# Kernel optimization log

Hardware: AMD Instinct MI355X
Metric: run time of the kernel (lower is better)

## Reference

```python
import jax, jax.numpy as jnp
import numpy as np

N = 50000      # nodes
E = 800000     # edges (avg degree 16)
F_IN = 256     # input feature dim
H, D = 4, 32   # heads, per-head dim
HD = H * D
K = 25000      # SAGPool keeps ceil(0.5*N) nodes
C = 2          # classes
SLOPE = 0.4
NEG = -1e9

def _gat(x, src, dst, valid, n, W, b, al, ar):
    # DGL GATConv: fc -> per-head attn logits -> edge softmax over dst -> weighted sum
    h = (x @ W).reshape(-1, H, D)                      # [n,H,D]
    el = jnp.einsum('nhd,hd->nh', h, al)
    er = jnp.einsum('nhd,hd->nh', h, ar)
    e = jax.nn.leaky_relu(el[src] + er[dst], SLOPE)    # [E,H]
    e = jnp.where(valid[:, None], e, NEG)
    m = jnp.maximum(jax.ops.segment_max(e, dst, num_segments=n), NEG)
    ex = jnp.exp(e - m[dst]) * valid[:, None].astype(x.dtype)
    s = jax.ops.segment_sum(ex, dst, num_segments=n)
    alpha = ex / jnp.maximum(s[dst], 1e-16)            # [E,H] edge softmax
    out = jax.ops.segment_sum(alpha[:, :, None] * h[src], dst, num_segments=n)
    return out + b.reshape(1, H, D), alpha

def _sagpool(x, src, dst, valid, n, k, Wc, bc):
    # score = GraphConv(in,1) with symmetric norm; keep top-k nodes, scale by tanh(score)
    vf = valid.astype(x.dtype)
    deg_o = jnp.maximum(jax.ops.segment_sum(vf, src, num_segments=n), 1.0)
    deg_i = jnp.maximum(jax.ops.segment_sum(vf, dst, num_segments=n), 1.0)
    h = (x @ Wc) * (deg_o ** -0.5)[:, None]
    agg = jax.ops.segment_sum(h[src] * vf[:, None], dst, num_segments=n)
    score = (agg * (deg_i ** -0.5)[:, None] + bc)[:, 0]   # [n]
    vals, perm = jax.lax.top_k(score, k)
    xk = x[perm] * jnp.tanh(vals)[:, None]                # [k,F]
    new_id = jnp.full((n,), -1, jnp.int32).at[perm].set(jnp.arange(k, dtype=jnp.int32))
    ns, nd = new_id[src], new_id[dst]
    nv = valid & (ns >= 0) & (nd >= 0)                    # edges fully inside subgraph
    return xk, jnp.where(nv, ns, 0), jnp.where(nv, nd, 0), nv

def setup_inputs():
    key = jax.random.key(0)
    k = jax.random.split(key, 18)
    rn = lambda i, shape, scale: jax.random.normal(k[i], shape, jnp.float32) * scale
    return {
        "feature": rn(0, (N, F_IN), 1.0),
        "strength": jax.random.uniform(k[1], (E,), dtype=jnp.float32),
        "W0": rn(2, (F_IN, HD), F_IN ** -0.5), "b0": jnp.zeros((HD,), jnp.float32),
        "al0": rn(3, (H, D), 0.1), "ar0": rn(4, (H, D), 0.1),
        "Wc0": rn(5, (HD, 1), HD ** -0.5), "bc0": jnp.zeros((1,), jnp.float32),
        "W1": rn(6, (HD, HD), HD ** -0.5), "b1": jnp.zeros((HD,), jnp.float32),
        "al1": rn(7, (H, D), 0.1), "ar1": rn(8, (H, D), 0.1),
        "gate_W": rn(9, (D, 1), D ** -0.5), "gate_b": jnp.zeros((1,), jnp.float32),
        "cls_W": rn(10, (D, C), D ** -0.5), "cls_b": jnp.zeros((C,), jnp.float32),
        "src": jax.random.randint(k[11], (E,), 0, N, dtype=jnp.int32),
        "dst": jax.random.randint(k[12], (E,), 0, N, dtype=jnp.int32),
    }

def reference(feature, strength, W0, b0, al0, ar0, Wc0, bc0, W1, b1, al1, ar1,
              gate_W, gate_b, cls_W, cls_b, src, dst):
    valid0 = jnp.ones((E,), bool)
    h0, _ = _gat(feature, src, dst, valid0, N, W0, b0, al0, ar0)
    x = h0.reshape(N, HD)                                  # flatten(1)
    x1, s1, d1, v1 = _sagpool(x, src, dst, valid0, N, K, Wc0, bc0)
    h1, atten = _gat(x1, s1, d1, v1, K, W1, b1, al1, ar1)  # get_attention=True
    strength1 = strength * v1.astype(strength.dtype)       # edata carried into subgraph (masked)
    res = h1.mean(axis=1)                                  # [K,D] mean over heads
    gate = jax.nn.softmax(res @ gate_W + gate_b, axis=0)   # [K,1] GlobalAttentionPooling
    readout = jnp.sum(gate * res, axis=0, keepdims=True)   # [1,D]
    lbl_pred = readout @ cls_W + cls_b                     # [1,C]
    return (readout, lbl_pred, atten, strength1)
```

## Files before the change

### kernel.cpp

```cpp
#include <hip/hip_runtime.h>
#include <stdint.h>

#define NN 50000
#define EE 800000
#define FIN 256
#define HD 128
#define DD 32
#define KK 25000
#define SLOPEF 0.4f
#define NEGF (-1e9f)
#define ATT_OFF 34
#define STR_OFF (34 + EE * 4)
#define CW 128

#define BCH 32
#define EPC (EE / BCH)

__device__ __forceinline__ unsigned fkey(float x) {
    unsigned u = __float_as_uint(x);
    return (u & 0x80000000u) ? ~u : (u | 0x80000000u);
}
__device__ __forceinline__ float unfkey(unsigned k) {
    unsigned u = (k & 0x80000000u) ? (k ^ 0x80000000u) : ~k;
    return __uint_as_float(u);
}
__device__ __forceinline__ float lrelu(float v) { return v > 0.f ? v : SLOPEF * v; }

struct P {
    const float *feature, *strength, *W0, *b0, *al0, *ar0, *Wc0, *bc0;
    const float *W1, *b1, *al1, *ar1, *gW, *gb, *cW, *cb;
    const int *src, *dst;
    double *Zacc, *racc;
    int *cnt;
    unsigned *gmaxk, *rs;
    unsigned *binsHi, *binsLo;
    unsigned *keys;
    unsigned char *degc_i, *degc_o, *degc1;
    unsigned *cb0, *cb1;
    int *dsum;
    int *ens, *end_;
    int *csr_src, *rank, *off0, *off1, *sel, *slot, *list, *bsum, *boff;
    float *z0, *el0, *er0, *q4, *m0f, *s0f, *b0wc, *hc, *score, *xk, *z1;
    float *el1, *er1, *m1f, *s1f, *res, *g, *tscale;
    float *out;
};

#define BM 128
#define BN 64
#define BK 16
__device__ void gemm_body(
    const float* __restrict__ A, const float* __restrict__ B, float* __restrict__ C,
    int M, int Kd,
    const float* __restrict__ al, const float* __restrict__ ar,
    float* __restrict__ el, float* __restrict__ er,
    const float* __restrict__ Wc, float* __restrict__ q4,
    int bx, int by) {
    __shared__ float As[BK][BM + 4];
    __shared__ float Bs[BK][BN];
    int bm = by * BM, bn = bx * BN;
    int tid = threadIdx.x;
    int tr = tid >> 4, tc = tid & 15;
    int lrow = tid >> 1;
    int arow = (bm + lrow < M) ? (bm + lrow) : -1;
    float acc[8][4] = {};
    for (int k0 = 0; k0 < Kd; k0 += BK) {
        {
            int col = (tid & 1) << 3;
            float4 v0 = {0.f,0.f,0.f,0.f}, v1 = {0.f,0.f,0.f,0.f};
            if (arow >= 0) {
                const float* ap = A + (size_t)arow * Kd + k0 + col;
                v0 = *(const float4*)ap; v1 = *(const float4*)(ap + 4);
            }
            As[col + 0][lrow] = v0.x; As[col + 1][lrow] = v0.y;
            As[col + 2][lrow] = v0.z; As[col + 3][lrow] = v0.w;
            As[col + 4][lrow] = v1.x; As[col + 5][lrow] = v1.y;
            As[col + 6][lrow] = v1.z; As[col + 7][lrow] = v1.w;
        }
        {
            int kr = tid >> 4, col = (tid & 15) << 2;
            float4 v = *(const float4*)(B + (size_t)(k0 + kr) * HD + bn + col);
            *(float4*)&Bs[kr][col] = v;
        }
        __syncthreads();
#pragma unroll
        for (int kk = 0; kk < BK; kk++) {
            float a[8], b[4];
#pragma unroll
            for (int i = 0; i < 8; i++) a[i] = As[kk][tr * 8 + i];
#pragma unroll
            for (int j = 0; j < 4; j++) b[j] = Bs[kk][tc * 4 + j];
#pragma unroll
            for (int i = 0; i < 8; i++)
#pragma unroll
                for (int j = 0; j < 4; j++) acc[i][j] = fmaf(a[i], b[j], acc[i][j]);
        }
        __syncthreads();
    }
#pragma unroll
    for (int i = 0; i < 8; i++) {
        int gr = bm + tr * 8 + i;
        if (gr < M) {
            float4 v = {acc[i][0], acc[i][1], acc[i][2], acc[i][3]};
            *(float4*)(C + (size_t)gr * HD + bn + tc * 4) = v;
        }
    }
    int head = bx * 2 + (tc >> 3);
    int dbase = (tc & 7) * 4;
    const float* alh = al + head * 32 + dbase;
    const float* arh = ar + head * 32 + dbase;
    float a0 = alh[0], a1 = alh[1], a2 = alh[2], a3 = alh[3];
    float r0 = arh[0], r1 = arh[1], r2 = arh[2], r3 = arh[3];
    float w0 = 0.f, w1 = 0.f, w2 = 0.f, w3 = 0.f;
    if (Wc) {
        const float* wch = Wc + head * 32 + dbase;
        w0 = wch[0]; w1 = wch[1]; w2 = wch[2]; w3 = wch[3];
    }
#pragma unroll
    for (int i = 0; i < 8; i++) {
        int gr = bm + tr * 8 + i;
        float pe = acc[i][0]*a0 + acc[i][1]*a1 + acc[i][2]*a2 + acc[i][3]*a3;
        float pr = acc[i][0]*r0 + acc[i][1]*r1 + acc[i][2]*r2 + acc[i][3]*r3;
        float pq = acc[i][0]*w0 + acc[i][1]*w1 + acc[i][2]*w2 + acc[i][3]*w3;
#pragma unroll
        for (int o = 1; o < 8; o <<= 1) {
            pe += __shfl_xor(pe, o); pr += __shfl_xor(pr, o); pq += __shfl_xor(pq, o);
        }
        if ((tc & 7) == 0 && gr < M) {
            el[gr * 4 + head] = pe; er[gr * 4 + head] = pr;
            if (Wc) q4[gr * 4 + head] = pq;
        }
    }
}

__global__ __launch_bounds__(256) void k_count0(P p) {
    __shared__ unsigned hist[NN / 4];
    int blk = blockIdx.x;
    int isD = blk < BCH;
    int c = isD ? blk : blk - BCH;
    for (int w = threadIdx.x; w < NN / 4; w += 256) hist[w] = 0u;
    __syncthreads();
    int j0 = c * EPC, j1 = j0 + EPC;
    if (isD) {
        for (int e = j0 + (int)threadIdx.x; e < j1; e += 256) {
            int d = p.dst[e];
            unsigned sh = (unsigned)(d & 3) * 8u;
            unsigned old = atomicAdd(&hist[d >> 2], 1u << sh);
            p.rank[e] = (int)((old >> sh) & 0xffu);
        }
    } else {
        for (int e = j0 + (int)threadIdx.x; e < j1; e += 256) {
            int s = p.src[e];
            atomicAdd(&hist[s >> 2], 1u << ((unsigned)(s & 3) * 8u));
        }
    }
    __syncthreads();
    unsigned* o32 = (unsigned*)((isD ? p.degc_i : p.degc_o) + (size_t)c * NN);
    for (int w = threadIdx.x; w < NN / 4; w += 256) o32[w] = hist[w];
}

__global__ __launch_bounds__(256) void k_count1(P p) {
    __shared__ unsigned hist[KK / 4];
    int c = blockIdx.x;
    for (int w = threadIdx.x; w < KK / 4; w += 256) hist[w] = 0u;
    __syncthreads();
    int j0 = c * EPC, j1 = j0 + EPC;
    for (int e = j0 + (int)threadIdx.x; e < j1; e += 256) {
        int d = p.end_[e];
        if (d >= 0) {
            unsigned sh = (unsigned)(d & 3) * 8u;
            unsigned old = atomicAdd(&hist[d >> 2], 1u << sh);
            p.rank[e] = (int)((old >> sh) & 0xffu);
        }
    }
    __syncthreads();
    unsigned* o32 = (unsigned*)(p.degc1 + (size_t)c * KK);
    for (int w = threadIdx.x; w < KK / 4; w += 256) o32[w] = hist[w];
}

__global__ void k_emap(P p) {
    int e = blockIdx.x * blockDim.x + threadIdx.x;
    if (e >= EE) return;
    int ns = p.slot[p.src[e]], nd = p.slot[p.dst[e]];
    if (ns < 0) nd = -1;
    p.ens[e] = ns;
    p.end_[e] = nd;
}

__global__ __launch_bounds__(256) void k_bsum(const unsigned char* __restrict__ deg,
                                              int* __restrict__ bsum, int n, int nn) {
    int i = blockIdx.x * 256 + threadIdx.x;
    int v = 0;
    if (i < n) {
#pragma unroll
        for (int c = 0; c < BCH; c++) v += deg[(size_t)c * nn + i];
    }
    int lane = threadIdx.x & 63, w = threadIdx.x >> 6;
    __shared__ int ws[4];
#pragma unroll
    for (int o = 1; o < 64; o <<= 1) v += __shfl_xor(v, o);
    if (lane == 0) ws[w] = v;
    __syncthreads();
    if (threadIdx.x == 0) bsum[blockIdx.x] = ws[0] + ws[1] + ws[2] + ws[3];
}
__global__ __launch_bounds__(256) void k_bscan(const int* __restrict__ bsum, int nb,
                                               int* __restrict__ boff,
                                               int* __restrict__ off, int n) {
    __shared__ int ws[4];
    __shared__ int wo[5];
    int t = threadIdx.x;
    int v = (t < nb) ? bsum[t] : 0;
    int lane = t & 63, w = t >> 6;
    int incl = v;
    for (int o = 1; o < 64; o <<= 1) { int u = __shfl_up(incl, o); if (lane >= o) incl += u; }
    if (lane == 63) ws[w] = incl;
    __syncthreads();
    if (t == 0) { int a = 0; for (int i = 0; i < 4; i++) { wo[i] = a; a += ws[i]; } wo[4] = a; }
    __syncthreads();
    if (t < nb) boff[t] = wo[w] + incl - v;
    if (t == 0) off[n] = wo[4];
}
__global__ __launch_bounds__(256) void k_fscan0(P p) {
    __shared__ int ws[4];
    __shared__ int wo[4];
    int i = blockIdx.x * 256 + threadIdx.x;
    int v = 0;
    if (i < NN) {
#pragma unroll
        for (int c = 0; c < BCH; c++) v += p.degc_i[(size_t)c * NN + i];
    }
    int lane = threadIdx.x & 63, w = threadIdx.x >> 6;
    int incl = v;
    for (int o = 1; o < 64; o <<= 1) { int u = __shfl_up(incl, o); if (lane >= o) incl += u; }
    if (lane == 63) ws[w] = incl;
    __syncthreads();
    if (threadIdx.x == 0) { int a = 0; for (int k = 0; k < 4; k++) { wo[k] = a; a += ws[k]; } }
    __syncthreads();
    if (i < NN) {
        int base = p.boff[blockIdx.x] + wo[w] + incl - v;
        p.off0[i] = base;
        unsigned run = (unsigned)base;
        int s = 0;
#pragma unroll
        for (int c = 0; c < BCH; c++) {
            p.cb0[(size_t)c * NN + i] = run;
            run += p.degc_i[(size_t)c * NN + i];
            s += p.degc_o[(size_t)c * NN + i];
        }
        p.dsum[i] = s;
    }
}
__global__ __launch_bounds__(256) void k_fscan1(P p) {
    __shared__ int ws[4];
    __shared__ int wo[4];
    int i = blockIdx.x * 256 + threadIdx.x;
    int v = 0;
    if (i < KK) {
#pragma unroll
        for (int c = 0; c < BCH; c++) v += p.degc1[(size_t)c * KK + i];
    }
    int lane = threadIdx.x & 63, w = threadIdx.x >> 6;
    int incl = v;
    for (int o = 1; o < 64; o <<= 1) { int u = __shfl_up(incl, o); if (lane >= o) incl += u; }
    if (lane == 63) ws[w] = incl;
    __syncthreads();
    if (threadIdx.x == 0) { int a = 0; for (int k = 0; k < 4; k++) { wo[k] = a; a += ws[k]; } }
    __syncthreads();
    if (i < KK) {
        int base = p.boff[blockIdx.x] + wo[w] + incl - v;
        p.off1[i] = base;
        unsigned run = (unsigned)base;
#pragma unroll
        for (int c = 0; c < BCH; c++) {
            p.cb1[(size_t)c * KK + i] = run;
            run += p.degc1[(size_t)c * KK + i];
        }
    }
}

#define G0B 782
#define GB_E 3125
__global__ __launch_bounds__(256) void k_g0sc(P p) {
    int blk = blockIdx.x;
    if (blk < G0B) {
        gemm_body(p.feature, p.W0, p.z0, NN, FIN, p.al0, p.ar0, p.el0, p.er0,
                  p.Wc0, p.q4, blk & 1, blk >> 1);
    } else if (blk < G0B + GB_E) {
        int e = (blk - G0B) * 256 + threadIdx.x;
        if (e < EE) {
            int c = e / EPC;
            int d = p.dst[e];
            unsigned pos = p.cb0[(size_t)c * NN + d] + (unsigned)p.rank[e];
            p.csr_src[pos] = p.src[e];
        }
    } else {
        int l = threadIdx.x;
        if (l < 64) {
            float t = p.b0[l] * p.Wc0[l] + p.b0[l + 64] * p.Wc0[l + 64];
#pragma unroll
            for (int o = 1; o < 64; o <<= 1) t += __shfl_xor(t, o);
            if (l == 0) p.b0wc[0] = t;
        }
    }
}

#define G1B 392
__global__ __launch_bounds__(256) void k_g1sc(P p) {
    int blk = blockIdx.x;
    if (blk < G1B) {
        gemm_body(p.xk, p.W1, p.z1, KK, HD, p.al1, p.ar1, p.el1, p.er1,
                  nullptr, nullptr, blk & 1, blk >> 1);
    } else {
        int e = (blk - G1B) * 256 + threadIdx.x;
        if (e < EE) {
            int d = p.end_[e];
            if (d >= 0) {
                int c = e / EPC;
                unsigned pos = p.cb1[(size_t)c * KK + d] + (unsigned)p.rank[e];
                p.csr_src[pos] = p.ens[e];
            }
        }
    }
}

__global__ __launch_bounds__(256) void k_fgatlite(
    const int* __restrict__ off, const int* __restrict__ csrs,
    const float* __restrict__ el, const float* __restrict__ er,
    const float* __restrict__ q4, const int* __restrict__ dsum,
    const float* __restrict__ b0wc,
    float* __restrict__ hc, float* __restrict__ m0f, float* __restrict__ s0f) {
    int wv = threadIdx.x >> 6, lane = threadIdx.x & 63;
    int v = blockIdx.x * 4 + wv;
    int b = off[v], e = off[v + 1], deg = e - b;
    int h = lane >> 4, sub = lane & 15;
    float erh = er[(size_t)v * 4 + h];
    float m = NEGF;
    for (int li = sub; li < deg; li += 16) {
        int s = csrs[b + li];
        m = fmaxf(m, lrelu(el[(size_t)s * 4 + h] + erh));
    }
#pragma unroll
    for (int o = 1; o < 16; o <<= 1) m = fmaxf(m, __shfl_xor(m, o));
    float ssum = 0.f, hq = 0.f;
    for (int li = sub; li < deg; li += 16) {
        int s = csrs[b + li];
        float ex = expf(lrelu(el[(size_t)s * 4 + h] + erh) - m);
        ssum += ex;
        hq = fmaf(ex, q4[(size_t)s * 4 + h], hq);
    }
#pragma unroll
    for (int o = 1; o < 16; o <<= 1) { ssum += __shfl_xor(ssum, o); hq += __shfl_xor(hq, o); }
    if (sub == 0) { m0f[v * 4 + h] = m; s0f[v * 4 + h] = ssum; }
    float t = hq / fmaxf(ssum, 1e-16f);
    t += __shfl_xor(t, 16);
    t += __shfl_xor(t, 32);
    if (lane == 0)
        hc[v] = (t + b0wc[0]) / sqrtf(fmaxf((float)dsum[v], 1.f));
}

__global__ __launch_bounds__(256) void k_fgatx(
    const int* __restrict__ list, const float* __restrict__ tscale,
    const int* __restrict__ off, const int* __restrict__ csrs,
    const float* __restrict__ el, const float* __restrict__ er,
    const float* __restrict__ m0f, const float* __restrict__ s0f,
    const float* __restrict__ z, const float* __restrict__ b0,
    float* __restrict__ xk) {
    __shared__ int ssrc[4][CW];
    __shared__ float sexp[4][CW][4];
    int wv = threadIdx.x >> 6, lane = threadIdx.x & 63;
    int i = blockIdx.x * 4 + wv;
    int v = list[i];
    int b = off[v], e = off[v + 1], deg = e - b;
    int h = lane >> 4, sub = lane & 15;
    float erh = er[(size_t)v * 4 + h];
    float mh = m0f[v * 4 + h];
    for (int li = sub; li < deg; li += 16) {
        int s = csrs[b + li];
        if (h == 0 && li < CW) ssrc[wv][li] = s;
        if (li < CW) sexp[wv][li][h] = expf(lrelu(el[(size_t)s * 4 + h] + erh) - mh);
    }
    __syncthreads();
    int h0 = lane >> 5, h1 = h0 + 2;
    float s0 = s0f[v * 4 + h0], s1 = s0f[v * 4 + h1];
    float m0 = m0f[v * 4 + h0], m1 = m0f[v * 4 + h1];
    float er0v = er[(size_t)v * 4 + h0], er1v = er[(size_t)v * 4 + h1];
    int c0 = lane, c1 = lane + 64;
    float acc0 = 0.f, acc1 = 0.f;
    for (int li = 0; li < deg; li++) {
        int s; float w0, w1;
        if (li < CW) {
            s = ssrc[wv][li];
            w0 = sexp[wv][li][h0]; w1 = sexp[wv][li][h1];
        } else {
            s = csrs[b + li];
            w0 = expf(lrelu(el[(size_t)s * 4 + h0] + er0v) - m0);
            w1 = expf(lrelu(el[(size_t)s * 4 + h1] + er1v) - m1);
        }
        int su = __builtin_amdgcn_readfirstlane(s);
        const float* zr = z + (size_t)su * HD;
        acc0 = fmaf(w0, zr[c0], acc0);
        acc1 = fmaf(w1, zr[c1], acc1);
    }
    float ts = tscale[i];
    float* xr = xk + (size_t)i * HD;
    xr[c0] = (acc0 / fmaxf(s0, 1e-16f) + b0[c0]) * ts;
    xr[c1] = (acc1 / fmaxf(s1, 1e-16f) + b0[c1]) * ts;
}

__global__ void k_score(P p) {
    int v = blockIdx.x * blockDim.x + threadIdx.x;
    if (v >= NN) return;
    int b = p.off0[v], en = p.off0[v + 1];
    float acc = 0.f;
    for (int i = b; i < en; i++) acc += p.hc[p.csr_src[i]];
    float dg = fmaxf((float)(en - b), 1.f);
    float sc = acc / sqrtf(dg) + p.bc0[0];
    p.score[v] = sc;
    p.keys[v] = fkey(sc);
}

__global__ void k_hist2(P p, int level) {
    int v = blockIdx.x * blockDim.x + threadIdx.x;
    if (v >= NN) return;
    unsigned key = p.keys[v];
    if (level == 0) atomicAdd(&p.binsHi[key >> 16], 1u);
    else if ((key >> 16) == p.rs[2]) atomicAdd(&p.binsLo[key & 0xFFFFu], 1u);
}
__global__ __launch_bounds__(1024) void k_rsel2(P p, int level) {
    const unsigned* bins = level ? p.binsLo : p.binsHi;
    int K = level ? (int)p.rs[3] : KK;
    __shared__ unsigned wsm[16];
    __shared__ unsigned wpre[17];
    int t = threadIdx.x;
    unsigned base = (unsigned)t * 64;
    const uint4* b4 = (const uint4*)(bins + base);
    unsigned S = 0;
#pragma unroll
    for (int i = 0; i < 16; i++) {
        uint4 u = b4[i];
        S += u.x + u.y + u.z + u.w;
    }
    int lane = t & 63, w = t >> 6;
    unsigned val = S;
    for (int o = 1; o < 64; o <<= 1) { unsigned u = __shfl_up(val, o); if (lane >= o) val += u; }
    if (lane == 63) wsm[w] = val;
    __syncthreads();
    if (t == 0) { unsigned a = 0; for (int i = 0; i < 16; i++) { wpre[i] = a; a += wsm[i]; } wpre[16] = a; }
    __syncthreads();
    unsigned incl = wpre[w] + val;
    unsigned running = wpre[16] - incl;
    for (int i = 63; i >= 0; i--) {
        unsigned c = bins[base + i];
        unsigned above = running;
        running += c;
        if ((int)above < K && (int)running >= K) {
            if (level == 0) { p.rs[2] = base + (unsigned)i; p.rs[3] = (unsigned)(K - (int)above); }
            else { p.rs[0] = (p.rs[2] << 16) | (base + (unsigned)i); p.rs[1] = (unsigned)(K - (int)above); }
        }
    }
}
__global__ void k_sel(P p) {
    int v = blockIdx.x * blockDim.x + threadIdx.x;
    if (v >= NN) return;
    p.sel[v] = (p.keys[v] > p.rs[0]) ? 1 : 0;
}
__global__ __launch_bounds__(1024) void k_ties(P p) {
    __shared__ int base;
    __shared__ int wsums[16];
    unsigned pivot = p.rs[0];
    int need = (int)p.rs[1];
    if (threadIdx.x == 0) base = 0;
    __syncthreads();
    for (int st = 0; st < NN; st += 1024) {
        int v = st + (int)threadIdx.x;
        int flag = (v < NN && p.keys[v] == pivot) ? 1 : 0;
        unsigned long long m = __ballot(flag);
        int lane = threadIdx.x & 63, w = threadIdx.x >> 6;
        int pre = __popcll(m & ((1ull << lane) - 1ull));
        if (lane == 0) wsums[w] = __popcll(m);
        __syncthreads();
        int woff = 0;
        for (int i = 0; i < w; i++) woff += wsums[i];
        int rank = base + woff + pre;
        if (flag && rank < need) p.sel[v] = 1;
        __syncthreads();
        if (threadIdx.x == 0) {
            int s = 0;
            for (int i = 0; i < 16; i++) s += wsums[i];
            base += s;
        }
        __syncthreads();
    }
}
__global__ void k_list(P p) {
    int v = blockIdx.x * blockDim.x + threadIdx.x;
    if (v >= NN) return;
    if (p.sel[v]) {
        int i = atomicAdd(p.cnt, 1);
        p.list[i] = v;
        p.slot[v] = i;
        p.tscale[i] = tanhf(p.score[v]);
    } else {
        p.slot[v] = -1;
    }
}

__global__ __launch_bounds__(256) void k_fgat2(
    const int* __restrict__ off, const int* __restrict__ csrs,
    const float* __restrict__ el, const float* __restrict__ er,
    const float* __restrict__ z, const float* __restrict__ bias,
    float* __restrict__ mf, float* __restrict__ sf,
    const float* __restrict__ gW, const float* __restrict__ gb,
    float* __restrict__ res, float* __restrict__ g) {
    __shared__ int ssrc[4][CW];
    __shared__ float sexp[4][CW][4];
    int wv = threadIdx.x >> 6, lane = threadIdx.x & 63;
    int v = blockIdx.x * 4 + wv;
    int b = off[v], e = off[v + 1], deg = e - b;
    int h = lane >> 4, sub = lane & 15;
    float4 er4 = *(const float4*)(er + (size_t)v * 4);
    float erh = ((const float*)&er4)[h];
    float m = NEGF;
    for (int li = sub; li < deg; li += 16) {
        int s = csrs[b + li];
        if (h == 0 && li < CW) ssrc[wv][li] = s;
        m = fmaxf(m, lrelu(el[(size_t)s * 4 + h] + erh));
    }
#pragma unroll
    for (int o = 1; o < 16; o <<= 1) m = fmaxf(m, __shfl_xor(m, o));
    float ssum = 0.f;
    for (int li = sub; li < deg; li += 16) {
        int s = csrs[b + li];
        float x = expf(lrelu(el[(size_t)s * 4 + h] + erh) - m);
        if (li < CW) sexp[wv][li][h] = x;
        ssum += x;
    }
#pragma unroll
    for (int o = 1; o < 16; o <<= 1) ssum += __shfl_xor(ssum, o);
    if (sub == 0) { mf[v * 4 + h] = m; sf[v * 4 + h] = ssum; }
    __syncthreads();
    int h0 = lane >> 5, h1 = h0 + 2;
    float m0 = __shfl(m, h0 << 4), m1 = __shfl(m, h1 << 4);
    float s0 = __shfl(ssum, h0 << 4), s1 = __shfl(ssum, h1 << 4);
    int c0 = lane, c1 = lane + 64;
    float acc0 = 0.f, acc1 = 0.f;
    for (int li = 0; li < deg; li++) {
        int s; float w0, w1;
        if (li < CW) {
            s = ssrc[wv][li];
            w0 = sexp[wv][li][h0]; w1 = sexp[wv][li][h1];
        } else {
            s = csrs[b + li];
            w0 = expf(lrelu(el[(size_t)s * 4 + h0] + ((const float*)&er4)[h0]) - m0);
            w1 = expf(lrelu(el[(size_t)s * 4 + h1] + ((const float*)&er4)[h1]) - m1);
        }
        int su = __builtin_amdgcn_readfirstlane(s);
        const float* zr = z + (size_t)su * HD;
        acc0 = fmaf(w0, zr[c0], acc0);
        acc1 = fmaf(w1, zr[c1], acc1);
    }
    float xc0 = acc0 / fmaxf(s0, 1e-16f) + bias[c0];
    float xc1 = acc1 / fmaxf(s1, 1e-16f) + bias[c1];
    float t = xc0 + xc1;
    t += __shfl_xor(t, 32);
    float pg = 0.f;
    if (lane < 32) {
        float r = 0.25f * t;
        res[(size_t)v * 32 + lane] = r;
        pg = r * gW[lane];
    }
#pragma unroll
    for (int o = 1; o < 32; o <<= 1) pg += __shfl_xor(pg, o);
    if (lane == 0) g[v] = pg + gb[0];
}

__global__ void k_ealpha1(P p) {
    int e = blockIdx.x * blockDim.x + threadIdx.x;
    if (e >= EE) return;
    int ds = p.ens[e], dd = p.end_[e];
    float a[4] = {0.f, 0.f, 0.f, 0.f};
    float st = 0.f;
    if (dd >= 0) {
        float4 es = *(const float4*)(p.el1 + ds * 4);
        float4 ed = *(const float4*)(p.er1 + dd * 4);
        float l[4] = {lrelu(es.x + ed.x), lrelu(es.y + ed.y), lrelu(es.z + ed.z), lrelu(es.w + ed.w)};
#pragma unroll
        for (int h = 0; h < 4; h++) {
            float m = p.m1f[dd * 4 + h];
            float ex = expf(l[h] - m);
            a[h] = ex / fmaxf(p.s1f[dd * 4 + h], 1e-16f);
        }
        st = p.strength[e];
    }
    float* o = p.out + ATT_OFF + (size_t)e * 4;
    *(float2*)(o) = make_float2(a[0], a[1]);
    *(float2*)(o + 2) = make_float2(a[2], a[3]);
    p.out[STR_OFF + e] = st;
}

__global__ void k_gmax(P p) {
    __shared__ float red[256];
    int t = threadIdx.x;
    float m = -3.4e38f;
    for (int i = blockIdx.x * 256 + t; i < KK; i += gridDim.x * 256) m = fmaxf(m, p.g[i]);
    red[t] = m;
    __syncthreads();
    for (int o = 128; o > 0; o >>= 1) { if (t < o) red[t] = fmaxf(red[t], red[t + o]); __syncthreads(); }
    if (t == 0) atomicMax(p.gmaxk, fkey(red[0]));
}
#define WSUM_BLOCKS 104
__global__ __launch_bounds__(256) void k_wsum(P p) {
    __shared__ double vred[256];
    __shared__ double zred[8];
    int t = threadIdx.x, il = t >> 5, d = t & 31;
    float gm = unfkey(*p.gmaxk);
    double accv = 0.0, accw = 0.0;
    for (int i = blockIdx.x * 8 + il; i < KK; i += WSUM_BLOCKS * 8) {
        float w = expf(p.g[i] - gm);
        accv += (double)(w * p.res[(size_t)i * 32 + d]);
        if (d == 0) accw += (double)w;
    }
    vred[t] = accv;
    if (d == 0) zred[il] = accw;
    __syncthreads();
    if (il == 0) {
        double s = 0;
#pragma unroll
        for (int k2 = 0; k2 < 8; k2++) s += vred[k2 * 32 + d];
        atomicAdd(&p.racc[d], s);
    }
    if (t == 32) {
        double z2 = 0;
#pragma unroll
        for (int k2 = 0; k2 < 8; k2++) z2 += zred[k2];
        atomicAdd(p.Zacc, z2);
    }
}
__global__ void k_final(P p) {
    __shared__ float rb[32];
    int t = threadIdx.x;
    double Z = *p.Zacc;
    if (t < 32) {
        float r = (float)(p.racc[t] / Z);
        p.out[t] = r;
        rb[t] = r;
    }
    __syncthreads();
    if (t < 2) {
        float s = 0.f;
        for (int d = 0; d < 32; d++) s += rb[d] * p.cW[d * 2 + t];
        p.out[32 + t] = s + p.cb[t];
    }
}

extern "C" void kernel_launch(void* const* d_in, const int* in_sizes, int n_in,
                              void* d_out, int out_size, void* d_ws, size_t ws_size,
                              hipStream_t stream) {
    (void)in_sizes; (void)n_in; (void)out_size; (void)ws_size;
    P p;
    p.feature  = (const float*)d_in[0];
    p.strength = (const float*)d_in[1];
    p.W0  = (const float*)d_in[2];  p.b0  = (const float*)d_in[3];
    p.al0 = (const float*)d_in[4];  p.ar0 = (const float*)d_in[5];
    p.Wc0 = (const float*)d_in[6];  p.bc0 = (const float*)d_in[7];
    p.W1  = (const float*)d_in[8];  p.b1  = (const float*)d_in[9];
    p.al1 = (const float*)d_in[10]; p.ar1 = (const float*)d_in[11];
    p.gW  = (const float*)d_in[12]; p.gb  = (const float*)d_in[13];
    p.cW  = (const float*)d_in[14]; p.cb  = (const float*)d_in[15];
    p.src = (const int*)d_in[16];   p.dst = (const int*)d_in[17];
    p.out = (float*)d_out;

    char* ws = (char*)d_ws;
    size_t off = 0;
    auto alloc = [&](size_t bytes) -> void* {
        void* r = ws + off;
        off = (off + bytes + 255) & ~(size_t)255;
        return r;
    };
    p.Zacc  = (double*)alloc(8);
    p.racc  = (double*)alloc(32 * 8);
    p.cnt   = (int*)alloc(4);
    p.gmaxk = (unsigned*)alloc(4);
    p.rs    = (unsigned*)alloc(16);
    p.binsHi = (unsigned*)alloc(65536 * 4);
    p.binsLo = (unsigned*)alloc(65536 * 4);
    size_t zbytes = off;
    p.degc_i = (unsigned char*)alloc((size_t)BCH * NN);
    p.degc_o = (unsigned char*)alloc((size_t)BCH * NN);
    p.degc1  = p.degc_i;
    p.cb0 = (unsigned*)alloc((size_t)BCH * NN * 4);
    p.cb1 = p.cb0;
    p.dsum = (int*)alloc((size_t)NN * 4);
    p.ens  = (int*)alloc((size_t)EE * 4);
    p.end_ = (int*)alloc((size_t)EE * 4);
    p.z0 = (float*)alloc((size_t)NN * HD * 4);
    p.xk = (float*)alloc((size_t)KK * HD * 4);
    p.z1 = (float*)alloc((size_t)KK * HD * 4);
    p.csr_src = (int*)alloc((size_t)EE * 4);
    p.rank    = (int*)alloc((size_t)EE * 4);
    p.el0 = (float*)alloc((size_t)NN * 4 * 4);
    p.er0 = (float*)alloc((size_t)NN * 4 * 4);
    p.q4  = (float*)alloc((size_t)NN * 4 * 4);
    p.m0f = (float*)alloc((size_t)NN * 4 * 4);
    p.s0f = (float*)alloc((size_t)NN * 4 * 4);
    p.b0wc = (float*)alloc(4);
    p.off0 = (int*)alloc((size_t)(NN + 1) * 4);
    p.off1 = (int*)alloc((size_t)(KK + 1) * 4);
    p.bsum = (int*)alloc(256 * 4);
    p.boff = (int*)alloc(256 * 4);
    p.hc    = (float*)alloc((size_t)NN * 4);
    p.score = (float*)alloc((size_t)NN * 4);
    p.keys  = (unsigned*)alloc((size_t)NN * 4);
    p.sel   = (int*)alloc((size_t)NN * 4);
    p.slot  = (int*)alloc((size_t)NN * 4);
    p.list  = (int*)alloc((size_t)KK * 4);
    p.tscale = (float*)alloc((size_t)KK * 4);
    p.el1 = (float*)alloc((size_t)KK * 4 * 4);
    p.er1 = (float*)alloc((size_t)KK * 4 * 4);
    p.m1f = (float*)alloc((size_t)KK * 4 * 4);
    p.s1f = (float*)alloc((size_t)KK * 4 * 4);
    p.res = (float*)alloc((size_t)KK * DD * 4);
    p.g   = (float*)alloc((size_t)KK * 4);

    const int GB_N = (NN + 255) / 256;
    const int GB_K = (KK + 255) / 256;

    hipMemsetAsync(d_ws, 0, zbytes, stream);

    k_count0<<<2 * BCH, 256, 0, stream>>>(p);
    k_bsum<<<GB_N, 256, 0, stream>>>(p.degc_i, p.bsum, NN, NN);
    k_bscan<<<1, 256, 0, stream>>>(p.bsum, GB_N, p.boff, p.off0, NN);
    k_fscan0<<<GB_N, 256, 0, stream>>>(p);
    k_g0sc<<<G0B + GB_E + 1, 256, 0, stream>>>(p);
    k_fgatlite<<<NN / 4, 256, 0, stream>>>(p.off0, p.csr_src, p.el0, p.er0, p.q4,
                                           p.dsum, p.b0wc, p.hc, p.m0f, p.s0f);

    k_score<<<GB_N, 256, 0, stream>>>(p);
    k_hist2<<<GB_N, 256, 0, stream>>>(p, 0);
    k_rsel2<<<1, 1024, 0, stream>>>(p, 0);
    k_hist2<<<GB_N, 256, 0, stream>>>(p, 1);
    k_rsel2<<<1, 1024, 0, stream>>>(p, 1);
    k_sel<<<GB_N, 256, 0, stream>>>(p);
    k_ties<<<1, 1024, 0, stream>>>(p);
    k_list<<<GB_N, 256, 0, stream>>>(p);

    k_emap<<<GB_E, 256, 0, stream>>>(p);
    k_count1<<<BCH, 256, 0, stream>>>(p);
    k_bsum<<<GB_K, 256, 0, stream>>>(p.degc1, p.bsum, KK, KK);
    k_bscan<<<1, 256, 0, stream>>>(p.bsum, GB_K, p.boff, p.off1, KK);
    k_fscan1<<<GB_K, 256, 0, stream>>>(p);
    k_fgatx<<<KK / 4, 256, 0, stream>>>(p.list, p.tscale, p.off0, p.csr_src,
                                        p.el0, p.er0, p.m0f, p.s0f, p.z0, p.b0, p.xk);
    k_g1sc<<<G1B + GB_E, 256, 0, stream>>>(p);
    k_fgat2<<<KK / 4, 256, 0, stream>>>(p.off1, p.csr_src, p.el1, p.er1, p.z1, p.b1,
                                        p.m1f, p.s1f, p.gW, p.gb, p.res, p.g);
    k_ealpha1<<<GB_E, 256, 0, stream>>>(p);

    k_gmax<<<98, 256, 0, stream>>>(p);
    k_wsum<<<WSUM_BLOCKS, 256, 0, stream>>>(p);
    k_final<<<1, 64, 0, stream>>>(p);
}
```

Baseline: 630.0 us.

## Fuse scans, top-k selection and readout into grid-barrier kernels; reuse level-0 CSR

Collapses many small launches into a few persistent kernels that use software grid barriers: the degree prefix scan, the whole SAGPool score/radix-select/tie/list pipeline, and the gate max/weighted-sum/final readout. It also drops the separate subgraph CSR build (emap, count1, scan1, scatter). The second GAT layer instead walks the level-0 CSR and filters sources through the slot map. This removes launch overhead and several serial single-block kernels. The cost is spin-wait barriers, which need every block to be co-resident, and extra slot lookups for dropped edges in the second layer.

Result: no change. 619.6 us (-1.6%).

```diff
diff --git a/kernel.cpp b/kernel.cpp
--- a/kernel.cpp
+++ b/kernel.cpp
@@ -26,20 +26,63 @@
 }
 __device__ __forceinline__ float lrelu(float v) { return v > 0.f ? v : SLOPEF * v; }
 
+__device__ __forceinline__ void ast(int* pp, int v) {
+    __hip_atomic_store(pp, v, __ATOMIC_RELAXED, __HIP_MEMORY_SCOPE_AGENT);
+}
+__device__ __forceinline__ int ald(const int* pp) {
+    return __hip_atomic_load(pp, __ATOMIC_RELAXED, __HIP_MEMORY_SCOPE_AGENT);
+}
+__device__ __forceinline__ void astu(unsigned* pp, unsigned v) {
+    __hip_atomic_store(pp, v, __ATOMIC_RELAXED, __HIP_MEMORY_SCOPE_AGENT);
+}
+__device__ __forceinline__ unsigned aldu(const unsigned* pp) {
+    return __hip_atomic_load(pp, __ATOMIC_RELAXED, __HIP_MEMORY_SCOPE_AGENT);
+}
+
+__device__ __forceinline__ void gridbar(int* cnt, int* flag, int nb) {
+    __syncthreads();
+    __threadfence();
+    if (threadIdx.x == 0) {
+        int old = __hip_atomic_fetch_add(cnt, 1, __ATOMIC_ACQ_REL, __HIP_MEMORY_SCOPE_AGENT);
+        if (old == nb - 1) {
+            __hip_atomic_store(flag, 1, __ATOMIC_RELEASE, __HIP_MEMORY_SCOPE_AGENT);
+        } else {
+            while (__hip_atomic_load(flag, __ATOMIC_ACQUIRE, __HIP_MEMORY_SCOPE_AGENT) == 0) {
+                __builtin_amdgcn_s_sleep(8);
+            }
+        }
+    }
+    __syncthreads();
+}
+
+__device__ __forceinline__ int blockscan(int v, int* lds) {
+    int lane = threadIdx.x & 63, w = threadIdx.x >> 6;
+    int incl = v;
+#pragma unroll
+    for (int o = 1; o < 64; o <<= 1) { int u = __shfl_up(incl, o); if (lane >= o) incl += u; }
+    __syncthreads();
+    if (lane == 63) lds[w] = incl;
+    __syncthreads();
+    int add = 0;
+    for (int i = 0; i < w; i++) add += lds[i];
+    return incl + add;
+}
+
 struct P {
     const float *feature, *strength, *W0, *b0, *al0, *ar0, *Wc0, *bc0;
     const float *W1, *b1, *al1, *ar1, *gW, *gb, *cW, *cb;
     const int *src, *dst;
     double *Zacc, *racc;
     int *cnt;
-    unsigned *gmaxk, *rs;
+    unsigned *gmaxk;
+    unsigned *rs;
+    int *bar;
     unsigned *binsHi, *binsLo;
     unsigned *keys;
-    unsigned char *degc_i, *degc_o, *degc1;
-    unsigned *cb0, *cb1;
+    unsigned char *degc_i, *degc_o;
+    unsigned *cb0;
     int *dsum;
-    int *ens, *end_;
-    int *csr_src, *rank, *off0, *off1, *sel, *slot, *list, *bsum, *boff;
+    int *csr_src, *rank, *off0, *sel, *slot, *list, *bsum;
     float *z0, *el0, *er0, *q4, *m0f, *s0f, *b0wc, *hc, *score, *xk, *z1;
     float *el1, *er1, *m1f, *s1f, *res, *g, *tscale;
     float *out;
@@ -158,85 +201,31 @@
     for (int w = threadIdx.x; w < NN / 4; w += 256) o32[w] = hist[w];
 }
 
-__global__ __launch_bounds__(256) void k_count1(P p) {
-    __shared__ unsigned hist[KK / 4];
-    int c = blockIdx.x;
-    for (int w = threadIdx.x; w < KK / 4; w += 256) hist[w] = 0u;
-    __syncthreads();
-    int j0 = c * EPC, j1 = j0 + EPC;
-    for (int e = j0 + (int)threadIdx.x; e < j1; e += 256) {
-        int d = p.end_[e];
-        if (d >= 0) {
-            unsigned sh = (unsigned)(d & 3) * 8u;
-            unsigned old = atomicAdd(&hist[d >> 2], 1u << sh);
-            p.rank[e] = (int)((old >> sh) & 0xffu);
-        }
-    }
-    __syncthreads();
-    unsigned* o32 = (unsigned*)(p.degc1 + (size_t)c * KK);
-    for (int w = threadIdx.x; w < KK / 4; w += 256) o32[w] = hist[w];
-}
-
-__global__ void k_emap(P p) {
-    int e = blockIdx.x * blockDim.x + threadIdx.x;
-    if (e >= EE) return;
-    int ns = p.slot[p.src[e]], nd = p.slot[p.dst[e]];
-    if (ns < 0) nd = -1;
-    p.ens[e] = ns;
-    p.end_[e] = nd;
-}
-
-__global__ __launch_bounds__(256) void k_bsum(const unsigned char* __restrict__ deg,
-                                              int* __restrict__ bsum, int n, int nn) {
-    int i = blockIdx.x * 256 + threadIdx.x;
-    int v = 0;
-    if (i < n) {
-#pragma unroll
-        for (int c = 0; c < BCH; c++) v += deg[(size_t)c * nn + i];
-    }
-    int lane = threadIdx.x & 63, w = threadIdx.x >> 6;
-    __shared__ int ws[4];
-#pragma unroll
-    for (int o = 1; o < 64; o <<= 1) v += __shfl_xor(v, o);
-    if (lane == 0) ws[w] = v;
-    __syncthreads();
-    if (threadIdx.x == 0) bsum[blockIdx.x] = ws[0] + ws[1] + ws[2] + ws[3];
-}
-__global__ __launch_bounds__(256) void k_bscan(const int* __restrict__ bsum, int nb,
-                                               int* __restrict__ boff,
-                                               int* __restrict__ off, int n) {
-    __shared__ int ws[4];
-    __shared__ int wo[5];
-    int t = threadIdx.x;
-    int v = (t < nb) ? bsum[t] : 0;
-    int lane = t & 63, w = t >> 6;
-    int incl = v;
-    for (int o = 1; o < 64; o <<= 1) { int u = __shfl_up(incl, o); if (lane >= o) incl += u; }
-    if (lane == 63) ws[w] = incl;
-    __syncthreads();
-    if (t == 0) { int a = 0; for (int i = 0; i < 4; i++) { wo[i] = a; a += ws[i]; } wo[4] = a; }
-    __syncthreads();
-    if (t < nb) boff[t] = wo[w] + incl - v;
-    if (t == 0) off[n] = wo[4];
-}
-__global__ __launch_bounds__(256) void k_fscan0(P p) {
-    __shared__ int ws[4];
-    __shared__ int wo[4];
-    int i = blockIdx.x * 256 + threadIdx.x;
-    int v = 0;
+#define SB 64
+__global__ __launch_bounds__(1024) void k_scan0(P p) {
+    __shared__ int lds[16];
+    __shared__ int ldsg[SB];
+    __shared__ int ldsb[2];
+    int tid = threadIdx.x, blk = blockIdx.x;
+    int i = blk * 1024 + tid;
+    int tot = 0;
     if (i < NN) {
 #pragma unroll
-        for (int c = 0; c < BCH; c++) v += p.degc_i[(size_t)c * NN + i];
-    }
-    int lane = threadIdx.x & 63, w = threadIdx.x >> 6;
-    int incl = v;
-    for (int o = 1; o < 64; o <<= 1) { int u = __shfl_up(incl, o); if (lane >= o) incl += u; }
-    if (lane == 63) ws[w] = incl;
-    __syncthreads();
-    if (threadIdx.x == 0) { int a = 0; for (int k = 0; k < 4; k++) { wo[k] = a; a += ws[k]; } }
+        for (int c = 0; c < BCH; c++) tot += p.degc_i[(size_t)c * NN + i];
+    }
+    int incl = blockscan(tot, lds);
+    if (tid == 1023) ast(&p.bsum[blk], incl);
+    gridbar(&p.bar[14], &p.bar[15], SB);
+    if (tid < SB) ldsg[tid] = ald(&p.bsum[tid]);
+    __syncthreads();
+    if (tid == 0) {
+        int pre = 0, all = 0;
+        for (int b2 = 0; b2 < SB; b2++) { if (b2 < blk) pre += ldsg[b2]; all += ldsg[b2]; }
+        ldsb[0] = pre; ldsb[1] = all;
+    }
     __syncthreads();
     if (i < NN) {
-        int base = p.boff[blockIdx.x] + wo[w] + incl - v;
+        int base = ldsb[0] + incl - tot;
         p.off0[i] = base;
         unsigned run = (unsigned)base;
         int s = 0;
@@ -248,33 +237,7 @@
         }
         p.dsum[i] = s;
     }
-}
-__global__ __launch_bounds__(256) void k_fscan1(P p) {
-    __shared__ int ws[4];
-    __shared__ int wo[4];
-    int i = blockIdx.x * 256 + threadIdx.x;
-    int v = 0;
-    if (i < KK) {
-#pragma unroll
-        for (int c = 0; c < BCH; c++) v += p.degc1[(size_t)c * KK + i];
-    }
-    int lane = threadIdx.x & 63, w = threadIdx.x >> 6;
-    int incl = v;
-    for (int o = 1; o < 64; o <<= 1) { int u = __shfl_up(incl, o); if (lane >= o) incl += u; }
-    if (lane == 63) ws[w] = incl;
-    __syncthreads();
-    if (threadIdx.x == 0) { int a = 0; for (int k = 0; k < 4; k++) { wo[k] = a; a += ws[k]; } }
-    __syncthreads();
-    if (i < KK) {
-        int base = p.boff[blockIdx.x] + wo[w] + incl - v;
-        p.off1[i] = base;
-        unsigned run = (unsigned)base;
-#pragma unroll
-        for (int c = 0; c < BCH; c++) {
-            p.cb1[(size_t)c * KK + i] = run;
-            run += p.degc1[(size_t)c * KK + i];
-        }
-    }
+    if (blk == 0 && tid == 0) p.off0[NN] = ldsb[1];
 }
 
 #define G0B 782
@@ -299,25 +262,6 @@
 #pragma unroll
             for (int o = 1; o < 64; o <<= 1) t += __shfl_xor(t, o);
             if (l == 0) p.b0wc[0] = t;
-        }
-    }
-}
-
-#define G1B 392
-__global__ __launch_bounds__(256) void k_g1sc(P p) {
-    int blk = blockIdx.x;
-    if (blk < G1B) {
-        gemm_body(p.xk, p.W1, p.z1, KK, HD, p.al1, p.ar1, p.el1, p.er1,
-                  nullptr, nullptr, blk & 1, blk >> 1);
-    } else {
-        int e = (blk - G1B) * 256 + threadIdx.x;
-        if (e < EE) {
-            int d = p.end_[e];
-            if (d >= 0) {
-                int c = e / EPC;
-                unsigned pos = p.cb1[(size_t)c * KK + d] + (unsigned)p.rank[e];
-                p.csr_src[pos] = p.ens[e];
-            }
         }
     }
 }
@@ -355,6 +299,101 @@
     t += __shfl_xor(t, 32);
     if (lane == 0)
         hc[v] = (t + b0wc[0]) / sqrtf(fmaxf((float)dsum[v], 1.f));
+}
+
+#define PB 64
+__global__ __launch_bounds__(1024) void k_pool(P p) {
+    __shared__ int lds[16];
+    __shared__ int ldsg[PB];
+    __shared__ int ldsb[2];
+    int tid = threadIdx.x, blk = blockIdx.x;
+    int gtid = blk * 1024 + tid;
+    if (gtid < NN) {
+        int b = p.off0[gtid], en = p.off0[gtid + 1];
+        float acc = 0.f;
+        for (int i = b; i < en; i++) acc += p.hc[p.csr_src[i]];
+        float dg = fmaxf((float)(en - b), 1.f);
+        float sc = acc / sqrtf(dg) + p.bc0[0];
+        p.score[gtid] = sc;
+        unsigned k_ = fkey(sc);
+        p.keys[gtid] = k_;
+        atomicAdd(&p.binsHi[k_ >> 16], 1u);
+    }
+    gridbar(&p.bar[0], &p.bar[1], PB);
+    {
+        int cnt = (int)p.binsHi[gtid];
+        int incl = blockscan(cnt, lds);
+        if (tid == 1023) ast(&p.bsum[64 + blk], incl);
+        gridbar(&p.bar[2], &p.bar[3], PB);
+        if (tid < PB) ldsg[tid] = ald(&p.bsum[64 + tid]);
+        __syncthreads();
+        if (tid == 0) {
+            int ab = 0;
+            for (int b2 = PB - 1; b2 > blk; b2--) ab += ldsg[b2];
+            ldsb[0] = ab; ldsb[1] = ldsg[blk];
+        }
+        __syncthreads();
+        int above = ldsb[0] + (ldsb[1] - incl);
+        if (above < KK && above + cnt >= KK) {
+            astu(&p.rs[64], (unsigned)gtid);
+            astu(&p.rs[65], (unsigned)(KK - above));
+        }
+    }
+    gridbar(&p.bar[4], &p.bar[5], PB);
+    unsigned hib = aldu(&p.rs[64]);
+    if (gtid < NN) {
+        unsigned k_ = p.keys[gtid];
+        if ((k_ >> 16) == hib) atomicAdd(&p.binsLo[k_ & 0xFFFFu], 1u);
+    }
+    gridbar(&p.bar[6], &p.bar[7], PB);
+    int K2 = (int)aldu(&p.rs[65]);
+    {
+        int cnt = (int)p.binsLo[gtid];
+        int incl = blockscan(cnt, lds);
+        if (tid == 1023) ast(&p.bsum[128 + blk], incl);
+        gridbar(&p.bar[8], &p.bar[9], PB);
+        if (tid < PB) ldsg[tid] = ald(&p.bsum[128 + tid]);
+        __syncthreads();
+        if (tid == 0) {
+            int ab = 0;
+            for (int b2 = PB - 1; b2 > blk; b2--) ab += ldsg[b2];
+            ldsb[0] = ab; ldsb[1] = ldsg[blk];
+        }
+        __syncthreads();
+        int above = ldsb[0] + (ldsb[1] - incl);
+        if (above < K2 && above + cnt >= K2) {
+            astu(&p.rs[0], (hib << 16) | (unsigned)gtid);
+            astu(&p.rs[1], (unsigned)(K2 - above));
+        }
+    }
+    gridbar(&p.bar[10], &p.bar[11], PB);
+    unsigned pivot = aldu(&p.rs[0]);
+    int need = (int)aldu(&p.rs[1]);
+    unsigned k_ = (gtid < NN) ? p.keys[gtid] : 0u;
+    int tie = (gtid < NN && k_ == pivot) ? 1 : 0;
+    int incl = blockscan(tie, lds);
+    if (tid == 1023) ast(&p.bsum[192 + blk], incl);
+    gridbar(&p.bar[12], &p.bar[13], PB);
+    if (tid < PB) ldsg[tid] = ald(&p.bsum[192 + tid]);
+    __syncthreads();
+    if (tid == 0) {
+        int pre = 0;
+        for (int b2 = 0; b2 < blk; b2++) pre += ldsg[b2];
+        ldsb[0] = pre;
+    }
+    __syncthreads();
+    int rank = ldsb[0] + incl - tie;
+    if (gtid < NN) {
+        int selv = (k_ > pivot) || (tie && rank < need);
+        if (selv) {
+            int idx = atomicAdd(p.cnt, 1);
+            p.list[idx] = gtid;
+            p.slot[gtid] = idx;
+            p.tscale[idx] = tanhf(p.score[gtid]);
+        } else {
+            p.slot[gtid] = -1;
+        }
+    }
 }
 
 __global__ __launch_bounds__(256) void k_fgatx(
@@ -406,137 +445,42 @@
     xr[c1] = (acc1 / fmaxf(s1, 1e-16f) + b0[c1]) * ts;
 }
 
-__global__ void k_score(P p) {
-    int v = blockIdx.x * blockDim.x + threadIdx.x;
-    if (v >= NN) return;
-    int b = p.off0[v], en = p.off0[v + 1];
-    float acc = 0.f;
-    for (int i = b; i < en; i++) acc += p.hc[p.csr_src[i]];
-    float dg = fmaxf((float)(en - b), 1.f);
-    float sc = acc / sqrtf(dg) + p.bc0[0];
-    p.score[v] = sc;
-    p.keys[v] = fkey(sc);
-}
-
-__global__ void k_hist2(P p, int level) {
-    int v = blockIdx.x * blockDim.x + threadIdx.x;
-    if (v >= NN) return;
-    unsigned key = p.keys[v];
-    if (level == 0) atomicAdd(&p.binsHi[key >> 16], 1u);
-    else if ((key >> 16) == p.rs[2]) atomicAdd(&p.binsLo[key & 0xFFFFu], 1u);
-}
-__global__ __launch_bounds__(1024) void k_rsel2(P p, int level) {
-    const unsigned* bins = level ? p.binsLo : p.binsHi;
-    int K = level ? (int)p.rs[3] : KK;
-    __shared__ unsigned wsm[16];
-    __shared__ unsigned wpre[17];
-    int t = threadIdx.x;
-    unsigned base = (unsigned)t * 64;
-    const uint4* b4 = (const uint4*)(bins + base);
-    unsigned S = 0;
-#pragma unroll
-    for (int i = 0; i < 16; i++) {
-        uint4 u = b4[i];
-        S += u.x + u.y + u.z + u.w;
-    }
-    int lane = t & 63, w = t >> 6;
-    unsigned val = S;
-    for (int o = 1; o < 64; o <<= 1) { unsigned u = __shfl_up(val, o); if (lane >= o) val += u; }
-    if (lane == 63) wsm[w] = val;
-    __syncthreads();
-    if (t == 0) { unsigned a = 0; for (int i = 0; i < 16; i++) { wpre[i] = a; a += wsm[i]; } wpre[16] = a; }
-    __syncthreads();
-    unsigned incl = wpre[w] + val;
-    unsigned running = wpre[16] - incl;
-    for (int i = 63; i >= 0; i--) {
-        unsigned c = bins[base + i];
-        unsigned above = running;
-        running += c;
-        if ((int)above < K && (int)running >= K) {
-            if (level == 0) { p.rs[2] = base + (unsigned)i; p.rs[3] = (unsigned)(K - (int)above); }
-            else { p.rs[0] = (p.rs[2] << 16) | (base + (unsigned)i); p.rs[1] = (unsigned)(K - (int)above); }
-        }
-    }
-}
-__global__ void k_sel(P p) {
-    int v = blockIdx.x * blockDim.x + threadIdx.x;
-    if (v >= NN) return;
-    p.sel[v] = (p.keys[v] > p.rs[0]) ? 1 : 0;
-}
-__global__ __launch_bounds__(1024) void k_ties(P p) {
-    __shared__ int base;
-    __shared__ int wsums[16];
-    unsigned pivot = p.rs[0];
-    int need = (int)p.rs[1];
-    if (threadIdx.x == 0) base = 0;
-    __syncthreads();
-    for (int st = 0; st < NN; st += 1024) {
-        int v = st + (int)threadIdx.x;
-        int flag = (v < NN && p.keys[v] == pivot) ? 1 : 0;
-        unsigned long long m = __ballot(flag);
-        int lane = threadIdx.x & 63, w = threadIdx.x >> 6;
-        int pre = __popcll(m & ((1ull << lane) - 1ull));
-        if (lane == 0) wsums[w] = __popcll(m);
-        __syncthreads();
-        int woff = 0;
-        for (int i = 0; i < w; i++) woff += wsums[i];
-        int rank = base + woff + pre;
-        if (flag && rank < need) p.sel[v] = 1;
-        __syncthreads();
-        if (threadIdx.x == 0) {
-            int s = 0;
-            for (int i = 0; i < 16; i++) s += wsums[i];
-            base += s;
-        }
-        __syncthreads();
-    }
-}
-__global__ void k_list(P p) {
-    int v = blockIdx.x * blockDim.x + threadIdx.x;
-    if (v >= NN) return;
-    if (p.sel[v]) {
-        int i = atomicAdd(p.cnt, 1);
-        p.list[i] = v;
-        p.slot[v] = i;
-        p.tscale[i] = tanhf(p.score[v]);
-    } else {
-        p.slot[v] = -1;
-    }
-}
-
-__global__ __launch_bounds__(256) void k_fgat2(
-    const int* __restrict__ off, const int* __restrict__ csrs,
-    const float* __restrict__ el, const float* __restrict__ er,
-    const float* __restrict__ z, const float* __restrict__ bias,
-    float* __restrict__ mf, float* __restrict__ sf,
-    const float* __restrict__ gW, const float* __restrict__ gb,
-    float* __restrict__ res, float* __restrict__ g) {
+#define G1B 392
+__global__ __launch_bounds__(256) void k_gemm1(P p) {
+    gemm_body(p.xk, p.W1, p.z1, KK, HD, p.al1, p.ar1, p.el1, p.er1,
+              nullptr, nullptr, blockIdx.x & 1, blockIdx.x >> 1);
+}
+
+__global__ __launch_bounds__(256) void k_fgat2(P p) {
     __shared__ int ssrc[4][CW];
     __shared__ float sexp[4][CW][4];
     int wv = threadIdx.x >> 6, lane = threadIdx.x & 63;
-    int v = blockIdx.x * 4 + wv;
-    int b = off[v], e = off[v + 1], deg = e - b;
+    int i = blockIdx.x * 4 + wv;
+    int v = p.list[i];
+    int b = p.off0[v], e = p.off0[v + 1], deg = e - b;
     int h = lane >> 4, sub = lane & 15;
-    float4 er4 = *(const float4*)(er + (size_t)v * 4);
+    float4 er4 = *(const float4*)(p.er1 + (size_t)i * 4);
     float erh = ((const float*)&er4)[h];
     float m = NEGF;
     for (int li = sub; li < deg; li += 16) {
-        int s = csrs[b + li];
-        if (h == 0 && li < CW) ssrc[wv][li] = s;
-        m = fmaxf(m, lrelu(el[(size_t)s * 4 + h] + erh));
+        int so = p.csr_src[b + li];
+        int ss = p.slot[so];
+        if (h == 0 && li < CW) ssrc[wv][li] = ss;
+        if (ss >= 0) m = fmaxf(m, lrelu(p.el1[(size_t)ss * 4 + h] + erh));
     }
 #pragma unroll
     for (int o = 1; o < 16; o <<= 1) m = fmaxf(m, __shfl_xor(m, o));
     float ssum = 0.f;
     for (int li = sub; li < deg; li += 16) {
-        int s = csrs[b + li];
-        float x = expf(lrelu(el[(size_t)s * 4 + h] + erh) - m);
+        int so = p.csr_src[b + li];
+        int ss = p.slot[so];
+        float x = (ss >= 0) ? expf(lrelu(p.el1[(size_t)ss * 4 + h] + erh) - m) : 0.f;
         if (li < CW) sexp[wv][li][h] = x;
         ssum += x;
     }
 #pragma unroll
     for (int o = 1; o < 16; o <<= 1) ssum += __shfl_xor(ssum, o);
-    if (sub == 0) { mf[v * 4 + h] = m; sf[v * 4 + h] = ssum; }
+    if (sub == 0) { p.m1f[i * 4 + h] = m; p.s1f[i * 4 + h] = ssum; }
     __syncthreads();
     int h0 = lane >> 5, h1 = h0 + 2;
     float m0 = __shfl(m, h0 << 4), m1 = __shfl(m, h1 << 4);
@@ -547,39 +491,42 @@
         int s; float w0, w1;
         if (li < CW) {
             s = ssrc[wv][li];
+            if (s < 0) continue;
             w0 = sexp[wv][li][h0]; w1 = sexp[wv][li][h1];
         } else {
-            s = csrs[b + li];
-            w0 = expf(lrelu(el[(size_t)s * 4 + h0] + ((const float*)&er4)[h0]) - m0);
-            w1 = expf(lrelu(el[(size_t)s * 4 + h1] + ((const float*)&er4)[h1]) - m1);
+            int so = p.csr_src[b + li];
+            s = p.slot[so];
+            if (s < 0) continue;
+            w0 = expf(lrelu(p.el1[(size_t)s * 4 + h0] + ((const float*)&er4)[h0]) - m0);
+            w1 = expf(lrelu(p.el1[(size_t)s * 4 + h1] + ((const float*)&er4)[h1]) - m1);
         }
         int su = __builtin_amdgcn_readfirstlane(s);
-        const float* zr = z + (size_t)su * HD;
+        const float* zr = p.z1 + (size_t)su * HD;
         acc0 = fmaf(w0, zr[c0], acc0);
         acc1 = fmaf(w1, zr[c1], acc1);
     }
-    float xc0 = acc0 / fmaxf(s0, 1e-16f) + bias[c0];
-    float xc1 = acc1 / fmaxf(s1, 1e-16f) + bias[c1];
+    float xc0 = acc0 / fmaxf(s0, 1e-16f) + p.b1[c0];
+    float xc1 = acc1 / fmaxf(s1, 1e-16f) + p.b1[c1];
     float t = xc0 + xc1;
     t += __shfl_xor(t, 32);
     float pg = 0.f;
     if (lane < 32) {
         float r = 0.25f * t;
-        res[(size_t)v * 32 + lane] = r;
-        pg = r * gW[lane];
+        p.res[(size_t)i * 32 + lane] = r;
+        pg = r * p.gW[lane];
     }
 #pragma unroll
     for (int o = 1; o < 32; o <<= 1) pg += __shfl_xor(pg, o);
-    if (lane == 0) g[v] = pg + gb[0];
+    if (lane == 0) p.g[i] = pg + p.gb[0];
 }
 
 __global__ void k_ealpha1(P p) {
     int e = blockIdx.x * blockDim.x + threadIdx.x;
     if (e >= EE) return;
-    int ds = p.ens[e], dd = p.end_[e];
+    int ds = p.slot[p.src[e]], dd = p.slot[p.dst[e]];
     float a[4] = {0.f, 0.f, 0.f, 0.f};
     float st = 0.f;
-    if (dd >= 0) {
+    if (ds >= 0 && dd >= 0) {
         float4 es = *(const float4*)(p.el1 + ds * 4);
         float4 ed = *(const float4*)(p.er1 + dd * 4);
         float l[4] = {lrelu(es.x + ed.x), lrelu(es.y + ed.y), lrelu(es.z + ed.z), lrelu(es.w + ed.w)};
@@ -597,24 +544,24 @@
     p.out[STR_OFF + e] = st;
 }
 
-__global__ void k_gmax(P p) {
-    __shared__ float red[256];
+#define RB 104
+__global__ __launch_bounds__(256) void k_read(P p) {
+    __shared__ float redf[256];
+    __shared__ double vred[256];
+    __shared__ double zred[8];
+    __shared__ float rb2[32];
     int t = threadIdx.x;
     float m = -3.4e38f;
-    for (int i = blockIdx.x * 256 + t; i < KK; i += gridDim.x * 256) m = fmaxf(m, p.g[i]);
-    red[t] = m;
-    __syncthreads();
-    for (int o = 128; o > 0; o >>= 1) { if (t < o) red[t] = fmaxf(red[t], red[t + o]); __syncthreads(); }
-    if (t == 0) atomicMax(p.gmaxk, fkey(red[0]));
-}
-#define WSUM_BLOCKS 104
-__global__ __launch_bounds__(256) void k_wsum(P p) {
-    __shared__ double vred[256];
-    __shared__ double zred[8];
-    int t = threadIdx.x, il = t >> 5, d = t & 31;
-    float gm = unfkey(*p.gmaxk);
+    for (int i = blockIdx.x * 256 + t; i < KK; i += RB * 256) m = fmaxf(m, p.g[i]);
+    redf[t] = m;
+    __syncthreads();
+    for (int o = 128; o > 0; o >>= 1) { if (t < o) redf[t] = fmaxf(redf[t], redf[t + o]); __syncthreads(); }
+    if (t == 0) atomicMax(p.gmaxk, fkey(redf[0]));
+    gridbar(&p.bar[16], &p.bar[17], RB);
+    int il = t >> 5, d = t & 31;
+    float gm = unfkey(aldu(p.gmaxk));
     double accv = 0.0, accw = 0.0;
-    for (int i = blockIdx.x * 8 + il; i < KK; i += WSUM_BLOCKS * 8) {
+    for (int i = blockIdx.x * 8 + il; i < KK; i += RB * 8) {
         float w = expf(p.g[i] - gm);
         accv += (double)(w * p.res[(size_t)i * 32 + d]);
         if (d == 0) accw += (double)w;
@@ -634,21 +581,20 @@
         for (int k2 = 0; k2 < 8; k2++) z2 += zred[k2];
         atomicAdd(p.Zacc, z2);
     }
-}
-__global__ void k_final(P p) {
-    __shared__ float rb[32];
-    int t = threadIdx.x;
-    double Z = *p.Zacc;
-    if (t < 32) {
-        float r = (float)(p.racc[t] / Z);
-        p.out[t] = r;
-        rb[t] = r;
-    }
-    __syncthreads();
-    if (t < 2) {
-        float s = 0.f;
-        for (int d = 0; d < 32; d++) s += rb[d] * p.cW[d * 2 + t];
-        p.out[32 + t] = s + p.cb[t];
+    gridbar(&p.bar[18], &p.bar[19], RB);
+    if (blockIdx.x == 0) {
+        double Z = *p.Zacc;
+        if (t < 32) {
+            float r = (float)(p.racc[t] / Z);
+            p.out[t] = r;
+            rb2[t] = r;
+        }
+        __syncthreads();
+        if (t < 2) {
+            float s = 0.f;
+            for (int dd2 = 0; dd2 < 32; dd2++) s += rb2[dd2] * p.cW[dd2 * 2 + t];
+            p.out[32 + t] = s + p.cb[t];
+        }
     }
 }
 
@@ -680,18 +626,15 @@
     p.racc  = (double*)alloc(32 * 8);
     p.cnt   = (int*)alloc(4);
     p.gmaxk = (unsigned*)alloc(4);
-    p.rs    = (unsigned*)alloc(16);
+    p.rs    = (unsigned*)alloc(128 * 4);
+    p.bar   = (int*)alloc(32 * 4);
     p.binsHi = (unsigned*)alloc(65536 * 4);
     p.binsLo = (unsigned*)alloc(65536 * 4);
     size_t zbytes = off;
     p.degc_i = (unsigned char*)alloc((size_t)BCH * NN);
     p.degc_o = (unsigned char*)alloc((size_t)BCH * NN);
-    p.degc1  = p.degc_i;
     p.cb0 = (unsigned*)alloc((size_t)BCH * NN * 4);
-    p.cb1 = p.cb0;
     p.dsum = (int*)alloc((size_t)NN * 4);
-    p.ens  = (int*)alloc((size_t)EE * 4);
-    p.end_ = (int*)alloc((size_t)EE * 4);
     p.z0 = (float*)alloc((size_t)NN * HD * 4);
     p.xk = (float*)alloc((size_t)KK * HD * 4);
     p.z1 = (float*)alloc((size_t)KK * HD * 4);
@@ -704,9 +647,7 @@
     p.s0f = (float*)alloc((size_t)NN * 4 * 4);
     p.b0wc = (float*)alloc(4);
     p.off0 = (int*)alloc((size_t)(NN + 1) * 4);
-    p.off1 = (int*)alloc((size_t)(KK + 1) * 4);
     p.bsum = (int*)alloc(256 * 4);
-    p.boff = (int*)alloc(256 * 4);
     p.hc    = (float*)alloc((size_t)NN * 4);
     p.score = (float*)alloc((size_t)NN * 4);
     p.keys  = (unsigned*)alloc((size_t)NN * 4);
@@ -721,41 +662,21 @@
     p.res = (float*)alloc((size_t)KK * DD * 4);
     p.g   = (float*)alloc((size_t)KK * 4);
 
-    const int GB_N = (NN + 255) / 256;
-    const int GB_K = (KK + 255) / 256;
-
     hipMemsetAsync(d_ws, 0, zbytes, stream);
 
     k_count0<<<2 * BCH, 256, 0, stream>>>(p);
-    k_bsum<<<GB_N, 256, 0, stream>>>(p.degc_i, p.bsum, NN, NN);
-    k_bscan<<<1, 256, 0, stream>>>(p.bsum, GB_N, p.boff, p.off0, NN);
-    k_fscan0<<<GB_N, 256, 0, stream>>>(p);
+    k_scan0<<<SB, 1024, 0, stream>>>(p);
     k_g0sc<<<G0B + GB_E + 1, 256, 0, stream>>>(p);
     k_fgatlite<<<NN / 4, 256, 0, stream>>>(p.off0, p.csr_src, p.el0, p.er0, p.q4,
                                            p.dsum, p.b0wc, p.hc, p.m0f, p.s0f);
 
-    k_score<<<GB_N, 256, 0, stream>>>(p);
-    k_hist2<<<GB_N, 256, 0, stream>>>(p, 0);
-    k_rsel2<<<1, 1024, 0, stream>>>(p, 0);
-    k_hist2<<<GB_N, 256, 0, stream>>>(p, 1);
-    k_rsel2<<<1, 1024, 0, stream>>>(p, 1);
-    k_sel<<<GB_N, 256, 0, stream>>>(p);
-    k_ties<<<1, 1024, 0, stream>>>(p);
-    k_list<<<GB_N, 256, 0, stream>>>(p);
-
-    k_emap<<<GB_E, 256, 0, stream>>>(p);
-    k_count1<<<BCH, 256, 0, stream>>>(p);
-    k_bsum<<<GB_K, 256, 0, stream>>>(p.degc1, p.bsum, KK, KK);
-    k_bscan<<<1, 256, 0, stream>>>(p.bsum, GB_K, p.boff, p.off1, KK);
-    k_fscan1<<<GB_K, 256, 0, stream>>>(p);
+    k_pool<<<PB, 1024, 0, stream>>>(p);
+
     k_fgatx<<<KK / 4, 256, 0, stream>>>(p.list, p.tscale, p.off0, p.csr_src,
                                         p.el0, p.er0, p.m0f, p.s0f, p.z0, p.b0, p.xk);
-    k_g1sc<<<G1B + GB_E, 256, 0, stream>>>(p);
-    k_fgat2<<<KK / 4, 256, 0, stream>>>(p.off1, p.csr_src, p.el1, p.er1, p.z1, p.b1,
-                                        p.m1f, p.s1f, p.gW, p.gb, p.res, p.g);
+    k_gemm1<<<G1B, 256, 0, stream>>>(p);
+    k_fgat2<<<KK / 4, 256, 0, stream>>>(p);
     k_ealpha1<<<GB_E, 256, 0, stream>>>(p);
 
-    k_gmax<<<98, 256, 0, stream>>>(p);
-    k_wsum<<<WSUM_BLOCKS, 256, 0, stream>>>(p);
-    k_final<<<1, 64, 0, stream>>>(p);
-}
+    k_read<<<RB, 256, 0, stream>>>(p);
+}
```
